# Kernel tuning notes

Hardware: AMD Instinct MI355X
Metric: run time of the kernel (lower is better)

The kernel has to match this reference:

```python
import jax, jax.numpy as jnp
import numpy as np

N, C, K, PARTS = 32, 256, 8192, 16
MAX_INIT = -100.0  # matches torch new_full((n,c,P), -100.0) with include_self=True


def setup_inputs() -> dict:
    key = jax.random.key(0)
    k1, k2, k3 = jax.random.split(key, 3)
    feats = jax.random.normal(k1, (N, C, K), dtype=jnp.float32)
    part_labels = jax.random.randint(k2, (K,), 0, PARTS, dtype=jnp.int64)
    valid_mask = jax.random.bernoulli(k3, 0.5, (N, K))
    return {"feats": feats, "part_labels": part_labels, "valid_mask": valid_mask}


def reference(feats, part_labels, valid_mask):
    n, c, k = feats.shape
    labels = part_labels.astype(jnp.int32)  # [k]
    vm = valid_mask.astype(feats.dtype)     # [n, k]

    # masked features for the mean branch (max branch uses raw feats, as in torch)
    valid_feat = feats * vm[:, None, :]      # [n, c, k]

    # scatter-add sum of valid features per part: [n, c, P]
    pooled_sum = jnp.zeros((n, c, PARTS), feats.dtype).at[:, :, labels].add(valid_feat)
    # scatter-add count of valid anchors per part: [n, P]
    pooled_count = jnp.zeros((n, PARTS), feats.dtype).at[:, labels].add(vm)
    # scatter-max over raw feats (unmasked, include_self with -100 init): [n, c, P]
    pooled_max = jnp.full((n, c, PARTS), MAX_INIT, feats.dtype).at[:, :, labels].max(feats)
    # anchors per part, independent of sample/mask: [P]
    patch_count = jnp.zeros((PARTS,), feats.dtype).at[labels].add(1.0)

    pooled_mean = pooled_sum / jnp.maximum(pooled_count, 1.0)[:, None, :]
    pooled_max = jnp.where(patch_count > 0, pooled_max, jnp.zeros_like(pooled_max))
    return pooled_mean + pooled_max  # [n, c, P]
```

## Files before the change

### kernel.cpp

```cpp
#include <hip/hip_runtime.h>

#define NN 32
#define CC 256
#define KK 8192
#define PARTS 16
#define TPB 256
#define PSTR 768
#define CH 16
#define NCH (CC / CH)
#define MAX_INIT (-100.0f)

typedef unsigned int uint32;
typedef unsigned short u16;


__global__ __launch_bounds__(TPB) void sortA(const int* __restrict__ labels,
                                             int* __restrict__ pcount,
                                             u16* __restrict__ permbase) {
    __shared__ u16 lh[PARTS * TPB];
    __shared__ u16 pexc[PARTS * TPB];
    __shared__ u16 wtot[PARTS][4];
    __shared__ u16 s_hist[PARTS];
    __shared__ __align__(16) u16 s_perm[PARTS * PSTR];
    const int t = threadIdx.x;
    const int w = t >> 6;
    const int lane = t & 63;

#pragma unroll
    for (int p = 0; p < PARTS; ++p) lh[p * TPB + t] = 0;
    int4 lv[8];
    const int4* l4 = (const int4*)labels + t * 8;
#pragma unroll
    for (int i = 0; i < 8; ++i) lv[i] = l4[i];
    __syncthreads();

#pragma unroll
    for (int i = 0; i < 8; ++i) {
        int la[4] = {lv[i].x, lv[i].y, lv[i].z, lv[i].w};
#pragma unroll
        for (int j = 0; j < 4; ++j) lh[(la[j] & 15) * TPB + t]++;
    }
    __syncthreads();

    for (int p = 0; p < PARTS; ++p) {
        uint32 v = lh[p * TPB + t];
        uint32 inc = v;
#pragma unroll
        for (int s = 1; s < 64; s <<= 1) {
            uint32 o = __shfl_up(inc, s, 64);
            if (lane >= s) inc += o;
        }
        pexc[p * TPB + t] = (u16)(inc - v);
        if (lane == 63) wtot[p][w] = (u16)inc;
    }
    __syncthreads();
    for (int p = 0; p < PARTS; ++p) {
        uint32 base = 0;
        for (int ww = 0; ww < w; ++ww) base += wtot[p][ww];
        pexc[p * TPB + t] = (u16)(pexc[p * TPB + t] + base);
    }
    __syncthreads();
    if (t < PARTS) s_hist[t] = (u16)(pexc[t * TPB + TPB - 1] + lh[t * TPB + TPB - 1]);
    __syncthreads();

#pragma unroll
    for (int p = 0; p < PARTS; ++p) lh[p * TPB + t] = 0;
#pragma unroll
    for (int i = 0; i < 8; ++i) {
        int la[4] = {lv[i].x, lv[i].y, lv[i].z, lv[i].w};
#pragma unroll
        for (int j = 0; j < 4; ++j) {
            int k = t * 32 + i * 4 + j;
            int p = la[j] & 15;
            u16 c = lh[p * TPB + t];
            uint32 q = (uint32)pexc[p * TPB + t] + c;
            lh[p * TPB + t] = (u16)(c + 1);
            if (q < PSTR) s_perm[p * PSTR + q] = (u16)k;
        }
    }
    __syncthreads();

    if (t < PARTS) {
        int p = t;
        uint32 beg = s_hist[p];
        u16 fill = (u16)((beg ? (s_perm[p * PSTR] & 0x1fffu) : 0u) | 0x4000u);
        for (uint32 q = beg; q < PSTR; ++q) s_perm[p * PSTR + q] = fill;
        pcount[p] = (int)s_hist[p];
    }
    __syncthreads();

    const uint4* src = (const uint4*)s_perm;
    uint4* dst = (uint4*)permbase;
#pragma unroll
    for (int j = 0; j < 6; ++j) dst[j * TPB + t] = src[j * TPB + t];
}

__global__ __launch_bounds__(TPB) void pool_kernel(const float* __restrict__ feats,
                                                   const u16* __restrict__ permbase,
                                                   const int* __restrict__ pcount,
                                                   const int* __restrict__ vm,
                                                   float* __restrict__ out) {
    __shared__ uint32 srow[2 * KK];
    const int t = threadIdx.x;
    const int blk = blockIdx.x;
    const int n = blk / NCH;
    const int c0 = (blk % NCH) * CH;
    const int w = t >> 6;
    const int lane = t & 63;
    const int g = t >> 4;
    const int l = t & 15;

    {
        const int4* vmn4 = (const int4*)(vm + (size_t)n * KK) + t * 8;
        uint32 bits = 0;
#pragma unroll
        for (int j = 0; j < 8; ++j) {
            int4 v = vmn4[j];
            bits |= (uint32)(v.x != 0) << (4 * j) | (uint32)(v.y != 0) << (4 * j + 1) |
                    (uint32)(v.z != 0) << (4 * j + 2) | (uint32)(v.w != 0) << (4 * j + 3);
        }
        srow[t] = bits;
    }

    uint32 pk[24];
    {
        const uint4* pb4 = (const uint4*)(permbase + g * PSTR + l * 48);
#pragma unroll
        for (int j = 0; j < 6; ++j) {
            uint4 q = pb4[j];
            pk[j * 4 + 0] = q.x;
            pk[j * 4 + 1] = q.y;
            pk[j * 4 + 2] = q.z;
            pk[j * 4 + 3] = q.w;
        }
    }
    __syncthreads();

    uint32 vb0 = 0, vb1 = 0;
#pragma unroll
    for (int i = 0; i < 48; ++i) {
        uint32 e = (pk[i >> 1] >> (16 * (i & 1))) & 0xffffu;
        uint32 k = e & 0x1fffu;
        uint32 valid = (e & 0x4000u) ? 0u : ((srow[k >> 5] >> (k & 31u)) & 1u);
        if (i < 32) vb0 |= valid << i;
        else        vb1 |= valid << (i - 32);
    }
    int cnt = __popc(vb0) + __popc(vb1);
#pragma unroll
    for (int m = 1; m < 16; m <<= 1) cnt += __shfl_xor(cnt, m, 16);
    const float cv = fmaxf((float)cnt, 1.0f);
    const int ph = pcount[g];
    __syncthreads();

    auto STAGE = [&](int buf, int r) {
        const float* frow = feats + (size_t)(n * CC + c0 + r) * KK;
#pragma unroll
        for (int i = 0; i < 8; ++i) {
            const int seg = w * 8 + i;
            __builtin_amdgcn_global_load_lds(
                (const __attribute__((address_space(1))) unsigned int*)(frow + seg * 256 + lane * 4),
                (__attribute__((address_space(3))) unsigned int*)&srow[buf * KK + seg * 256],
                16, 0, 0);
        }
    };

    STAGE(0, 0);
    for (int r = 0; r < CH; ++r) {
        const int cur = r & 1;
        const bool more = (r + 1 < CH);
        if (more) {
            STAGE(cur ^ 1, r + 1);
            asm volatile("s_waitcnt vmcnt(8)" ::: "memory");
        } else {
            asm volatile("s_waitcnt vmcnt(0)" ::: "memory");
        }
        __builtin_amdgcn_s_barrier();

        const uint32* rowp = &srow[cur * KK];
        float rs0 = 0.0f, rs1 = 0.0f;
        float rm0 = MAX_INIT, rm1 = MAX_INIT;
#pragma unroll
        for (int i = 0; i < 48; ++i) {
            uint32 k = (pk[i >> 1] >> (16 * (i & 1))) & 0x1fffu;
            float f = __uint_as_float(rowp[k]);
            uint32 vb = (i < 32) ? vb0 : vb1;
            uint32 sel = (vb >> (i & 31u)) & 1u;
            if (i & 1) { rm1 = fmaxf(rm1, f); rs1 += sel ? f : 0.0f; }
            else       { rm0 = fmaxf(rm0, f); rs0 += sel ? f : 0.0f; }
        }
        float rs = rs0 + rs1;
        float rm = fmaxf(rm0, rm1);
#pragma unroll
        for (int m = 1; m < 16; m <<= 1) {
            rs += __shfl_xor(rs, m, 16);
            rm = fmaxf(rm, __shfl_xor(rm, m, 16));
        }
        if (l == 0)
            out[(size_t)(n * CC + c0 + r) * PARTS + g] = rs / cv + (ph > 0 ? rm : 0.0f);

        if (more) __builtin_amdgcn_s_barrier();
    }
}

extern "C" void kernel_launch(void* const* d_in, const int* in_sizes, int n_in,
                              void* d_out, int out_size, void* d_ws, size_t ws_size,
                              hipStream_t stream) {
    const float* feats  = (const float*)d_in[0];
    const int*   labels = (const int*)d_in[1];
    const int*   vm     = (const int*)d_in[2];
    float* out = (float*)d_out;

    int* pcount   = (int*)d_ws;
    u16* permbase = (u16*)((char*)d_ws + 64);

    sortA<<<1, TPB, 0, stream>>>(labels, pcount, permbase);
    pool_kernel<<<NN * NCH, TPB, 0, stream>>>(feats, permbase, pcount, vm, out);
}
```

Baseline: 67.23 us.

## Deepen feature-row LDS pipeline to four buffers and precompute gather offsets/masks

The pool kernel goes from double to quadruple buffering of feature rows in LDS (128 KB), keeping three rows of async global-to-LDS loads in flight. The inner gather loop now uses precomputed byte offsets and float masks with FMA and four accumulator chains, replacing the per-element bit extraction. The sort kernel also spreads its padding fill across all threads instead of 16. The extra LDS and the launch-bounds hint of one block limit occupancy to one block per CU, which trades parallelism for deeper per-block prefetch, and the 96 extra registers per thread risk spills.

```diff
diff --git a/kernel.cpp b/kernel.cpp
--- a/kernel.cpp
+++ b/kernel.cpp
@@ -80,12 +80,13 @@
     }
     __syncthreads();
 
-    if (t < PARTS) {
-        int p = t;
+    {
+        const int p = t >> 4;
+        const int idx = t & 15;
         uint32 beg = s_hist[p];
         u16 fill = (u16)((beg ? (s_perm[p * PSTR] & 0x1fffu) : 0u) | 0x4000u);
-        for (uint32 q = beg; q < PSTR; ++q) s_perm[p * PSTR + q] = fill;
-        pcount[p] = (int)s_hist[p];
+        for (uint32 q = beg + idx; q < PSTR; q += 16) s_perm[p * PSTR + q] = fill;
+        if (t < PARTS) pcount[t] = (int)s_hist[t];
     }
     __syncthreads();
 
@@ -95,12 +96,12 @@
     for (int j = 0; j < 6; ++j) dst[j * TPB + t] = src[j * TPB + t];
 }
 
-__global__ __launch_bounds__(TPB) void pool_kernel(const float* __restrict__ feats,
-                                                   const u16* __restrict__ permbase,
-                                                   const int* __restrict__ pcount,
-                                                   const int* __restrict__ vm,
-                                                   float* __restrict__ out) {
-    __shared__ uint32 srow[2 * KK];
+__global__ __launch_bounds__(TPB, 1) void pool_kernel(const float* __restrict__ feats,
+                                                      const u16* __restrict__ permbase,
+                                                      const int* __restrict__ pcount,
+                                                      const int* __restrict__ vm,
+                                                      float* __restrict__ out) {
+    __shared__ uint32 srow[4 * KK];
     const int t = threadIdx.x;
     const int blk = blockIdx.x;
     const int n = blk / NCH;
@@ -136,16 +137,18 @@
     }
     __syncthreads();
 
-    uint32 vb0 = 0, vb1 = 0;
+    uint32 ga[48];
+    float gm[48];
+    int cnt = 0;
 #pragma unroll
     for (int i = 0; i < 48; ++i) {
         uint32 e = (pk[i >> 1] >> (16 * (i & 1))) & 0xffffu;
         uint32 k = e & 0x1fffu;
         uint32 valid = (e & 0x4000u) ? 0u : ((srow[k >> 5] >> (k & 31u)) & 1u);
-        if (i < 32) vb0 |= valid << i;
-        else        vb1 |= valid << (i - 32);
-    }
-    int cnt = __popc(vb0) + __popc(vb1);
+        ga[i] = k * 4u;
+        gm[i] = valid ? 1.0f : 0.0f;
+        cnt += (int)valid;
+    }
 #pragma unroll
     for (int m = 1; m < 16; m <<= 1) cnt += __shfl_xor(cnt, m, 16);
     const float cv = fmaxf((float)cnt, 1.0f);
@@ -165,31 +168,41 @@
     };
 
     STAGE(0, 0);
+    STAGE(1, 1);
+    STAGE(2, 2);
     for (int r = 0; r < CH; ++r) {
-        const int cur = r & 1;
-        const bool more = (r + 1 < CH);
-        if (more) {
-            STAGE(cur ^ 1, r + 1);
+        if (r + 3 < CH) {
+            STAGE((r + 3) & 3, r + 3);
+            asm volatile("s_waitcnt vmcnt(24)" ::: "memory");
+        } else if (r + 2 < CH) {
+            asm volatile("s_waitcnt vmcnt(16)" ::: "memory");
+        } else if (r + 1 < CH) {
             asm volatile("s_waitcnt vmcnt(8)" ::: "memory");
         } else {
             asm volatile("s_waitcnt vmcnt(0)" ::: "memory");
         }
         __builtin_amdgcn_s_barrier();
 
-        const uint32* rowp = &srow[cur * KK];
-        float rs0 = 0.0f, rs1 = 0.0f;
-        float rm0 = MAX_INIT, rm1 = MAX_INIT;
-#pragma unroll
-        for (int i = 0; i < 48; ++i) {
-            uint32 k = (pk[i >> 1] >> (16 * (i & 1))) & 0x1fffu;
-            float f = __uint_as_float(rowp[k]);
-            uint32 vb = (i < 32) ? vb0 : vb1;
-            uint32 sel = (vb >> (i & 31u)) & 1u;
-            if (i & 1) { rm1 = fmaxf(rm1, f); rs1 += sel ? f : 0.0f; }
-            else       { rm0 = fmaxf(rm0, f); rs0 += sel ? f : 0.0f; }
-        }
-        float rs = rs0 + rs1;
-        float rm = fmaxf(rm0, rm1);
+        const char* rowb = (const char*)&srow[(r & 3) * KK];
+        float rs0 = 0.0f, rs1 = 0.0f, rs2 = 0.0f, rs3 = 0.0f;
+        float rm0 = MAX_INIT, rm1 = MAX_INIT, rm2 = MAX_INIT, rm3 = MAX_INIT;
+#pragma unroll
+        for (int i = 0; i < 48; i += 4) {
+            float f0 = *(const float*)(rowb + ga[i]);
+            float f1 = *(const float*)(rowb + ga[i + 1]);
+            float f2 = *(const float*)(rowb + ga[i + 2]);
+            float f3 = *(const float*)(rowb + ga[i + 3]);
+            rm0 = fmaxf(rm0, f0);
+            rs0 = fmaf(f0, gm[i], rs0);
+            rm1 = fmaxf(rm1, f1);
+            rs1 = fmaf(f1, gm[i + 1], rs1);
+            rm2 = fmaxf(rm2, f2);
+            rs2 = fmaf(f2, gm[i + 2], rs2);
+            rm3 = fmaxf(rm3, f3);
+            rs3 = fmaf(f3, gm[i + 3], rs3);
+        }
+        float rs = (rs0 + rs1) + (rs2 + rs3);
+        float rm = fmaxf(fmaxf(rm0, rm1), fmaxf(rm2, rm3));
 #pragma unroll
         for (int m = 1; m < 16; m <<= 1) {
             rs += __shfl_xor(rs, m, 16);
@@ -198,7 +211,7 @@
         if (l == 0)
             out[(size_t)(n * CC + c0 + r) * PARTS + g] = rs / cv + (ph > 0 ? rm : 0.0f);
 
-        if (more) __builtin_amdgcn_s_barrier();
+        __builtin_amdgcn_s_barrier();
     }
 }
 
```

New measurement: 76.29 us. +13.5%, slower.
